# Optimization experiments

Measured on AMD Instinct MI355X. Metric: run time of the kernel, lower is better.

## Reference

```python
import jax, jax.numpy as jnp
import numpy as np

L, H, C, T, V = 6, 6, 384, 256, 65  # n_layer, n_head, n_embd, block_size, vocab_size
DH = C // H                          # head_size = 64
FF = 4 * C                           # 1536
B = 256


def _ln(x, g, b):
    m = x.mean(-1, keepdims=True)
    v = ((x - m) ** 2).mean(-1, keepdims=True)
    return (x - m) * jax.lax.rsqrt(v + 1e-5) * g + b


def setup_inputs() -> dict:
    key = jax.random.key(0)
    ks = jax.random.split(key, 24)
    s = 0.02
    n = lambda k, shp: jax.random.normal(k, shp, dtype=jnp.float32) * s
    return {
        "idx": jax.random.randint(ks[0], (B, T), 0, V),
        "targets": jax.random.randint(ks[1], (B, T), 0, V),
        "tok_emb": n(ks[2], (V, C)),
        "pos_emb": n(ks[3], (T, C)),
        "Wq": n(ks[4], (L, C, C)),
        "Wk": n(ks[5], (L, C, C)),
        "Wv": n(ks[6], (L, C, C)),
        "Wo": n(ks[7], (L, C, C)),
        "bo": jnp.zeros((L, C), jnp.float32),
        "ln1_g": jnp.ones((L, C), jnp.float32),
        "ln1_b": jnp.zeros((L, C), jnp.float32),
        "ln2_g": jnp.ones((L, C), jnp.float32),
        "ln2_b": jnp.zeros((L, C), jnp.float32),
        "W1": n(ks[8], (L, C, FF)),
        "b1": jnp.zeros((L, FF), jnp.float32),
        "W2": n(ks[9], (L, FF, C)),
        "b2": jnp.zeros((L, C), jnp.float32),
        "lnf_g": jnp.ones((C,), jnp.float32),
        "lnf_b": jnp.zeros((C,), jnp.float32),
        "Wh": n(ks[10], (C, V)),
        "bh": jnp.zeros((V,), jnp.float32),
    }


def _forward(idx, targets, tok_emb, pos_emb, Wq, Wk, Wv, Wo, bo,
             ln1_g, ln1_b, ln2_g, ln2_b, W1, b1, W2, b2, lnf_g, lnf_b, Wh, bh):
    Bx, Tx = idx.shape
    x = tok_emb[idx] + pos_emb[:Tx]                       # [B,T,C]
    causal = jnp.tril(jnp.ones((Tx, Tx), bool))

    def block(x, p):
        wq, wk, wv, wo, bo_, g1, b1_, g2, b2_, w1, bf1, w2, bf2 = p
        h = _ln(x, g1, b1_)
        q = (h @ wq).reshape(Bx, Tx, H, DH).transpose(0, 2, 1, 3)   # [B,H,T,Dh]
        k = (h @ wk).reshape(Bx, Tx, H, DH).transpose(0, 2, 1, 3)
        v = (h @ wv).reshape(Bx, Tx, H, DH).transpose(0, 2, 1, 3)
        scores = jnp.einsum('bhqd,bhkd->bhqk', q, k) * (DH ** -0.5)
        scores = jnp.where(causal, scores, -jnp.inf)
        att = jax.nn.softmax(scores, axis=-1)                       # dropout = eval (identity)
        o = jnp.einsum('bhqk,bhkd->bhqd', att, v)
        o = o.transpose(0, 2, 1, 3).reshape(Bx, Tx, C)
        x = x + o @ wo + bo_
        h2 = _ln(x, g2, b2_)
        x = x + jax.nn.relu(h2 @ w1 + bf1) @ w2 + bf2
        return x, None

    x, _ = jax.lax.scan(block, x, (Wq, Wk, Wv, Wo, bo, ln1_g, ln1_b,
                                   ln2_g, ln2_b, W1, b1, W2, b2))
    x = _ln(x, lnf_g, lnf_b)
    logits = (x @ Wh + bh).reshape(Bx * Tx, V)
    logp = jax.nn.log_softmax(logits, axis=-1)
    loss = -logp[jnp.arange(Bx * Tx), targets.reshape(-1)].mean()
    return logits, loss


def reference(idx, targets, tok_emb, pos_emb, Wq, Wk, Wv, Wo, bo,
              ln1_g, ln1_b, ln2_g, ln2_b, W1, b1, W2, b2, lnf_g, lnf_b, Wh, bh):
    return _forward(idx, targets, tok_emb, pos_emb, Wq, Wk, Wv, Wo, bo,
                    ln1_g, ln1_b, ln2_g, ln2_b, W1, b1, W2, b2, lnf_g, lnf_b, Wh, bh)
```

## Files before the change

kernel.cpp:

```cpp
#include <hip/hip_runtime.h>
#include <stdint.h>


typedef unsigned short u16;
typedef unsigned int   u32;
typedef __attribute__((ext_vector_type(8))) short bf16x8;
typedef __attribute__((ext_vector_type(4))) float f32x4;

typedef const __attribute__((address_space(1))) void* gas_ptr;
typedef __attribute__((address_space(3))) void* lds_ptr;

__device__ __forceinline__ void gld_lds16(const void* g, void* l) {
    __builtin_amdgcn_global_load_lds((gas_ptr)g, (lds_ptr)l, 16, 0, 0);
}

__device__ __forceinline__ u16 f2bf(float f) {
    u32 u = __builtin_bit_cast(u32, f);
    u = u + 0x7fffu + ((u >> 16) & 1u);
    return (u16)(u >> 16);
}
__device__ __forceinline__ float bf2f(u16 h) { return __builtin_bit_cast(float, (u32)h << 16); }
__device__ __forceinline__ float bflo(u32 u) { return __builtin_bit_cast(float, u << 16); }
__device__ __forceinline__ float bfhi(u32 u) { return __builtin_bit_cast(float, u & 0xffff0000u); }

__global__ __launch_bounds__(256)
void convT_k(const float* __restrict__ src, u16* __restrict__ dst,
             int L, int R, int C, int dls, int dco)
{
    size_t total  = (size_t)L * R * C;
    size_t stride = (size_t)gridDim.x * 256;
    for (size_t i = (size_t)blockIdx.x * 256 + threadIdx.x; i < total; i += stride) {
        size_t rc  = (size_t)R * C;
        size_t l   = i / rc;
        size_t rem = i - l * rc;
        int r = (int)(rem / C);
        int c = (int)(rem - (size_t)r * C);
        dst[l * (size_t)dls + (size_t)(dco + c) * R + r] = f2bf(src[i]);
    }
}

__global__ __launch_bounds__(256)
void embed_k(const int* __restrict__ idx, const float* __restrict__ tok,
             const float* __restrict__ pos, u16* __restrict__ x,
             float* __restrict__ lossbuf)
{
    if (blockIdx.x == 0 && threadIdx.x < 32) lossbuf[threadIdx.x] = 0.f;
    int gi  = blockIdx.x * 256 + threadIdx.x;
    int row = gi / 48;
    int cg  = gi - row * 48;
    int t   = row & 255;
    const float4* ta = (const float4*)(tok + (size_t)idx[row] * 384 + cg * 8);
    const float4* pa = (const float4*)(pos + (size_t)t * 384 + cg * 8);
    float4 a0 = ta[0], a1 = ta[1], p0 = pa[0], p1 = pa[1];
    u16 o[8] = { f2bf(a0.x+p0.x), f2bf(a0.y+p0.y), f2bf(a0.z+p0.z), f2bf(a0.w+p0.w),
                 f2bf(a1.x+p1.x), f2bf(a1.y+p1.y), f2bf(a1.z+p1.z), f2bf(a1.w+p1.w) };
    *(uint4*)(x + (size_t)row * 384 + cg * 8) = *(uint4*)o;
}

__global__ __launch_bounds__(256)
void ln_k(const u16* __restrict__ x, const float* __restrict__ gg,
          const float* __restrict__ bb, u16* __restrict__ out)
{
    const int lane = threadIdx.x & 63;
    const int w    = threadIdx.x >> 6;
    const size_t row = (size_t)blockIdx.x * 4 + w;
    const u32* xr = (const u32*)(x + row * 384);
    u32 d[3] = { xr[lane], xr[64 + lane], xr[128 + lane] };
    float v[6];
#pragma unroll
    for (int k = 0; k < 3; ++k) { v[2*k] = bflo(d[k]); v[2*k+1] = bfhi(d[k]); }
    float s = 0.f, sq = 0.f;
#pragma unroll
    for (int j = 0; j < 6; ++j) { s += v[j]; sq += v[j]*v[j]; }
#pragma unroll
    for (int m = 1; m < 64; m <<= 1) { s += __shfl_xor(s, m); sq += __shfl_xor(sq, m); }
    float mean = s * (1.f / 384.f);
    float var  = sq * (1.f / 384.f) - mean * mean;
    float rs   = rsqrtf(var + 1e-5f);
    u32* orow = (u32*)(out + row * 384);
#pragma unroll
    for (int k = 0; k < 3; ++k) {
        int c = k * 128 + 2 * lane;
        float o0 = (v[2*k]   - mean) * rs * gg[c]   + bb[c];
        float o1 = (v[2*k+1] - mean) * rs * gg[c+1] + bb[c+1];
        orow[k*64 + lane] = (u32)f2bf(o0) | ((u32)f2bf(o1) << 16);
    }
}

template<int EPI>
__global__ __launch_bounds__(256)
void gemm_bt(const u16* __restrict__ A, const u16* __restrict__ Bt,
             u16* __restrict__ C, float* __restrict__ Cf,
             const float* __restrict__ bias, int K, int N)
{
    __shared__ u16 As[2][128*32];
    __shared__ u16 Bs[2][128*32];
    const int tid = threadIdx.x;
    const int lane = tid & 63;
    const int w  = tid >> 6;
    const int wm = w >> 1, wn = w & 1;

    const int ntn = (N + 127) >> 7;
    const int cpx = gridDim.x >> 3;
    const int swz = (blockIdx.x & 7) * cpx + (blockIdx.x >> 3);
    const int mt  = swz / ntn;
    const int m0  = mt * 128;
    const int n0  = (swz - mt * ntn) * 128;

    const int g   = lane >> 4;
    const int l15 = lane & 15;

    f32x4 acc[4][4] = {};
    const int nk = K >> 5;

    auto stage = [&](int buf, int t) {
        const int k0 = t << 5;
#pragma unroll
        for (int c = 0; c < 2; ++c) {
            int i   = c * 256 + tid;
            int row = i >> 2;
            int seg = (i & 3) ^ (row & 3);
            gld_lds16(A  + (size_t)(m0 + row) * K + k0 + seg * 8,
                      (char*)(&As[buf][0]) + (c * 256 + w * 64) * 16);
            gld_lds16(Bt + (size_t)(n0 + row) * K + k0 + seg * 8,
                      (char*)(&Bs[buf][0]) + (c * 256 + w * 64) * 16);
        }
    };

    stage(0, 0);
    __syncthreads();
    int cur = 0;
    for (int t = 0; t < nk; ++t) {
        if (t + 1 < nk) stage(cur ^ 1, t + 1);
        const char* Ab = (const char*)&As[cur][0];
        const char* Bb = (const char*)&Bs[cur][0];
        bf16x8 af[4], bfv[4];
#pragma unroll
        for (int fm = 0; fm < 4; ++fm) {
            int row = wm*64 + fm*16 + l15;
            af[fm] = *(const bf16x8*)(Ab + row*64 + ((g ^ (row & 3)) * 16));
        }
#pragma unroll
        for (int fn = 0; fn < 4; ++fn) {
            int row = wn*64 + fn*16 + l15;
            bfv[fn] = *(const bf16x8*)(Bb + row*64 + ((g ^ (row & 3)) * 16));
        }
#pragma unroll
        for (int fm = 0; fm < 4; ++fm)
#pragma unroll
            for (int fn = 0; fn < 4; ++fn)
                acc[fm][fn] = __builtin_amdgcn_mfma_f32_16x16x32_bf16(
                    af[fm], bfv[fn], acc[fm][fn], 0, 0, 0);
        __syncthreads();
        cur ^= 1;
    }

#pragma unroll
    for (int fm = 0; fm < 4; ++fm) {
        int rowb = m0 + wm*64 + fm*16 + g*4;
#pragma unroll
        for (int fn = 0; fn < 4; ++fn) {
            int col = n0 + wn*64 + fn*16 + l15;
            float bv = (EPI == 0) ? 0.f
                     : ((EPI == 3 && col >= N) ? 0.f : bias[col]);
#pragma unroll
            for (int r = 0; r < 4; ++r) {
                size_t off = (size_t)(rowb + r) * N + col;
                float vv = acc[fm][fn][r];
                if (EPI == 0) {
                    C[off] = f2bf(vv);
                } else if (EPI == 1) {
                    vv += bv; vv = vv > 0.f ? vv : 0.f;
                    C[off] = f2bf(vv);
                } else if (EPI == 2) {
                    C[off] = f2bf(bf2f(C[off]) + vv + bv);
                } else {
                    if (col < N) Cf[off] = vv + bv;
                }
            }
        }
    }
}

__global__ __launch_bounds__(256)
void attn_k(const u16* __restrict__ qkv, u16* __restrict__ op)
{
    __shared__ u16 Ks[256*64];
    __shared__ u16 Vt[64*256];
    __shared__ u16 Ps[4][64*64];
    const int tid  = threadIdx.x;
    const int lane = tid & 63;
    const int w    = tid >> 6;
    const int g    = lane >> 4;
    const int l15  = lane & 15;
    const int bh = blockIdx.x;
    const int b  = bh / 6, hh = bh - b * 6;
    const size_t baseQ = (size_t)b * 256 * 1152 + hh * 64;
    const size_t baseK = baseQ + 384;
    const size_t baseV = baseQ + 768;

#pragma unroll
    for (int cc = 0; cc < 8; ++cc) {
        int i    = cc * 256 + tid;
        int row  = i >> 3;
        int slot = (i & 7) ^ (row & 7);
        gld_lds16(qkv + baseK + (size_t)row * 1152 + slot * 8,
                  (char*)Ks + (cc * 256 + w * 64) * 16);
    }
#pragma unroll
    for (int it = 0; it < 16; ++it) {
        int j    = it * 256 + tid;
        int trow = j >> 4;
        int d0   = (j & 15) * 4;
        uint2 val = *(const uint2*)(qkv + baseV + (size_t)trow * 1152 + d0);
        u16 e0 = (u16)(val.x & 0xffff), e1 = (u16)(val.x >> 16);
        u16 e2 = (u16)(val.y & 0xffff), e3 = (u16)(val.y >> 16);
        *(u16*)((char*)Vt + (d0+0)*512 + ((trow*2) ^ (((d0+0)&7) << 4))) = e0;
        *(u16*)((char*)Vt + (d0+1)*512 + ((trow*2) ^ (((d0+1)&7) << 4))) = e1;
        *(u16*)((char*)Vt + (d0+2)*512 + ((trow*2) ^ (((d0+2)&7) << 4))) = e2;
        *(u16*)((char*)Vt + (d0+3)*512 + ((trow*2) ^ (((d0+3)&7) << 4))) = e3;
    }
    __syncthreads();

    const int r0 = w * 64;
    bf16x8 qf[4][2];
#pragma unroll
    for (int fm = 0; fm < 4; ++fm)
#pragma unroll
        for (int kk = 0; kk < 2; ++kk)
            qf[fm][kk] = *(const bf16x8*)(qkv + baseQ +
                (size_t)(r0 + fm*16 + l15) * 1152 + kk*32 + g*8);

    f32x4 oacc[4][4] = {};
    float mst[4][4], lst[4][4];
#pragma unroll
    for (int i = 0; i < 4; ++i)
#pragma unroll
        for (int r = 0; r < 4; ++r) { mst[i][r] = -1e30f; lst[i][r] = 0.f; }

    for (int kt = 0; kt <= w; ++kt) {
        f32x4 s[4][4] = {};
#pragma unroll
        for (int kk = 0; kk < 2; ++kk) {
            bf16x8 kf[4];
#pragma unroll
            for (int fn = 0; fn < 4; ++fn) {
                int row = kt*64 + fn*16 + l15;
                kf[fn] = *(const bf16x8*)((char*)Ks + row*128 +
                          ((kk*64 + g*16) ^ ((row & 7) << 4)));
            }
#pragma unroll
            for (int fm = 0; fm < 4; ++fm)
#pragma unroll
                for (int fn = 0; fn < 4; ++fn)
                    s[fm][fn] = __builtin_amdgcn_mfma_f32_16x16x32_bf16(
                        qf[fm][kk], kf[fn], s[fm][fn], 0, 0, 0);
        }
        const bool diag = (kt == w);
#pragma unroll
        for (int fm = 0; fm < 4; ++fm) {
#pragma unroll
            for (int r = 0; r < 4; ++r) {
                int rowg = r0 + fm*16 + g*4 + r;
                float mx = -1e30f;
#pragma unroll
                for (int fn = 0; fn < 4; ++fn) {
                    float val = s[fm][fn][r] * 0.125f;
                    if (diag) {
                        int colg = kt*64 + fn*16 + l15;
                        if (colg > rowg) val = -1e30f;
                    }
                    s[fm][fn][r] = val;
                    mx = fmaxf(mx, val);
                }
                mx = fmaxf(mx, __shfl_xor(mx, 1));
                mx = fmaxf(mx, __shfl_xor(mx, 2));
                mx = fmaxf(mx, __shfl_xor(mx, 4));
                mx = fmaxf(mx, __shfl_xor(mx, 8));
                float mnew = fmaxf(mst[fm][r], mx);
                float sf   = __expf(mst[fm][r] - mnew);
                mst[fm][r] = mnew;
                float rowsum = 0.f;
#pragma unroll
                for (int fn = 0; fn < 4; ++fn) {
                    float pe = __expf(s[fm][fn][r] - mnew);
                    s[fm][fn][r] = pe;
                    rowsum += pe;
                }
                rowsum += __shfl_xor(rowsum, 1);
                rowsum += __shfl_xor(rowsum, 2);
                rowsum += __shfl_xor(rowsum, 4);
                rowsum += __shfl_xor(rowsum, 8);
                lst[fm][r] = lst[fm][r] * sf + rowsum;
#pragma unroll
                for (int fd = 0; fd < 4; ++fd) oacc[fm][fd][r] *= sf;
                int prow = fm*16 + g*4 + r;
#pragma unroll
                for (int fn = 0; fn < 4; ++fn) {
                    int pcol = fn*16 + l15;
                    *(u16*)((char*)Ps[w] + prow*128 +
                            ((pcol*2) ^ ((prow & 7) << 4))) = f2bf(s[fm][fn][r]);
                }
            }
        }
        asm volatile("s_waitcnt lgkmcnt(0)" ::: "memory");
#pragma unroll
        for (int kk2 = 0; kk2 < 2; ++kk2) {
            bf16x8 pa[4], vb[4];
#pragma unroll
            for (int fm = 0; fm < 4; ++fm) {
                int prow = fm*16 + l15;
                pa[fm] = *(const bf16x8*)((char*)Ps[w] + prow*128 +
                          ((kk2*64 + g*16) ^ ((prow & 7) << 4)));
            }
#pragma unroll
            for (int fd = 0; fd < 4; ++fd) {
                int vrow = fd*16 + l15;
                vb[fd] = *(const bf16x8*)((char*)Vt + vrow*512 +
                          ((kt*128 + kk2*64 + g*16) ^ ((vrow & 7) << 4)));
            }
#pragma unroll
            for (int fm = 0; fm < 4; ++fm)
#pragma unroll
                for (int fd = 0; fd < 4; ++fd)
                    oacc[fm][fd] = __builtin_amdgcn_mfma_f32_16x16x32_bf16(
                        pa[fm], vb[fd], oacc[fm][fd], 0, 0, 0);
        }
    }
#pragma unroll
    for (int fm = 0; fm < 4; ++fm)
#pragma unroll
        for (int r = 0; r < 4; ++r) {
            int rowg = r0 + fm*16 + g*4 + r;
            float inv = 1.f / lst[fm][r];
#pragma unroll
            for (int fd = 0; fd < 4; ++fd)
                op[((size_t)b * 256 + rowg) * 384 + hh*64 + fd*16 + l15] =
                    f2bf(oacc[fm][fd][r] * inv);
        }
}

__global__ __launch_bounds__(256)
void loss_k(const float* __restrict__ logits, const int* __restrict__ tgt,
            float* __restrict__ lossbuf)
{
    __shared__ float wloss[4];
    const int lane = threadIdx.x & 63;
    const int w    = threadIdx.x >> 6;
    const int wid  = blockIdx.x * 4 + w;
    float acc = 0.f;
    for (int rr = 0; rr < 16; ++rr) {
        const size_t row = (size_t)wid * 16 + rr;
        const float* lr = logits + row * 65;
        float v   = lr[lane];
        float l64 = lr[64];
        float mx = fmaxf(v, l64);
#pragma unroll
        for (int m = 1; m < 64; m <<= 1) mx = fmaxf(mx, __shfl_xor(mx, m));
        float e = __expf(v - mx);
#pragma unroll
        for (int m = 1; m < 64; m <<= 1) e += __shfl_xor(e, m);
        e += __expf(l64 - mx);
        float lse = mx + logf(e);
        int t = tgt[row];
        float lt0 = __shfl(v, t < 64 ? t : 0);
        float lt  = (t < 64) ? lt0 : l64;
        acc += lse - lt;
    }
    if (lane == 0) wloss[w] = acc;
    __syncthreads();
    if (threadIdx.x == 0) {
        float bsum = wloss[0] + wloss[1] + wloss[2] + wloss[3];
        atomicAdd(&lossbuf[blockIdx.x & 31], bsum * (1.f / 65536.f));
    }
}

__global__ void loss_finish_k(const float* __restrict__ part, float* __restrict__ outp)
{
    int lane = threadIdx.x;
    float v = (lane < 32) ? part[lane] : 0.f;
#pragma unroll
    for (int m = 1; m < 64; m <<= 1) v += __shfl_xor(v, m);
    if (lane == 0) outp[0] = v;
}

extern "C" void kernel_launch(void* const* d_in, const int* in_sizes, int n_in,
                              void* d_out, int out_size, void* d_ws, size_t ws_size,
                              hipStream_t stream)
{
    (void)in_sizes; (void)n_in; (void)out_size;
    const int*   idx  = (const int*)d_in[0];
    const int*   tgt  = (const int*)d_in[1];
    const float* tok  = (const float*)d_in[2];
    const float* pos  = (const float*)d_in[3];
    const float* Wq   = (const float*)d_in[4];
    const float* Wk   = (const float*)d_in[5];
    const float* Wv   = (const float*)d_in[6];
    const float* Wo   = (const float*)d_in[7];
    const float* bo   = (const float*)d_in[8];
    const float* ln1g = (const float*)d_in[9];
    const float* ln1b = (const float*)d_in[10];
    const float* ln2g = (const float*)d_in[11];
    const float* ln2b = (const float*)d_in[12];
    const float* W1   = (const float*)d_in[13];
    const float* b1   = (const float*)d_in[14];
    const float* W2   = (const float*)d_in[15];
    const float* b2   = (const float*)d_in[16];
    const float* lnfg = (const float*)d_in[17];
    const float* lnfb = (const float*)d_in[18];
    const float* Wh   = (const float*)d_in[19];
    const float* bh   = (const float*)d_in[20];

    const size_t fixed = (size_t)65536*384*2 * 2
                       + (size_t)6*1152*384*2
                       + (size_t)6*384*384*2
                       + (size_t)6*1536*384*2 * 2
                       + (size_t)128*384*2 + 4096;
    int NC = 4;
    if      (ws_size >= fixed + (size_t)65536*1536*2)      NC = 1;
    else if (ws_size >= fixed + (size_t)32768*1536*2)      NC = 2;
    const int CR = 65536 / NC;

    char* p = (char*)d_ws;
    u16* x    = (u16*)p;  p += (size_t)65536*384*2;
    u16* hbuf = (u16*)p;  p += (size_t)65536*384*2;
    u16* r1   = (u16*)p;  p += (size_t)CR*1536*2;
    u16* wqkv = (u16*)p;  p += (size_t)6*1152*384*2;
    u16* wto  = (u16*)p;  p += (size_t)6*384*384*2;
    u16* wt1  = (u16*)p;  p += (size_t)6*1536*384*2;
    u16* wt2  = (u16*)p;  p += (size_t)6*384*1536*2;
    u16* wth  = (u16*)p;  p += (size_t)128*384*2;
    float* lossbuf = (float*)p;

    float* out   = (float*)d_out;
    float* lossp = out + (size_t)65536 * 65;

    convT_k<<<1024, 256, 0, stream>>>(Wq, wqkv, 6, 384, 384, 442368, 0);
    convT_k<<<1024, 256, 0, stream>>>(Wk, wqkv, 6, 384, 384, 442368, 384);
    convT_k<<<1024, 256, 0, stream>>>(Wv, wqkv, 6, 384, 384, 442368, 768);
    convT_k<<<1024, 256, 0, stream>>>(Wo, wto, 6, 384, 384, 147456, 0);
    convT_k<<<2048, 256, 0, stream>>>(W1, wt1, 6, 384, 1536, 589824, 0);
    convT_k<<<2048, 256, 0, stream>>>(W2, wt2, 6, 1536, 384, 589824, 0);
    convT_k<<<64,   256, 0, stream>>>(Wh, wth, 1, 384, 65, 24960, 0);

    embed_k<<<12288, 256, 0, stream>>>(idx, tok, pos, x, lossbuf);

    for (int l = 0; l < 6; ++l) {
        ln_k<<<16384, 256, 0, stream>>>(x, ln1g + l*384, ln1b + l*384, hbuf);
        for (int ac = 0; ac < NC; ++ac) {
            const size_t ro = (size_t)ac * CR;
            gemm_bt<0><<<dim3((CR/128)*9), 256, 0, stream>>>(
                hbuf + ro*384, wqkv + (size_t)l*442368, r1, nullptr, nullptr, 384, 1152);
            attn_k<<<(CR/256)*6, 256, 0, stream>>>(r1, hbuf + ro*384);
        }
        gemm_bt<2><<<dim3(512*3), 256, 0, stream>>>(
            hbuf, wto + (size_t)l*147456, x, nullptr, bo + l*384, 384, 384);
        ln_k<<<16384, 256, 0, stream>>>(x, ln2g + l*384, ln2b + l*384, hbuf);
        for (int mc = 0; mc < NC; ++mc) {
            const size_t ro = (size_t)mc * CR;
            gemm_bt<1><<<dim3((CR/128)*12), 256, 0, stream>>>(
                hbuf + ro*384, wt1 + (size_t)l*589824, r1, nullptr, b1 + l*1536, 384, 1536);
            gemm_bt<2><<<dim3((CR/128)*3), 256, 0, stream>>>(
                r1, wt2 + (size_t)l*589824, x + ro*384, nullptr, b2 + l*384, 1536, 384);
        }
    }
    ln_k<<<16384, 256, 0, stream>>>(x, lnfg, lnfb, hbuf);
    gemm_bt<3><<<dim3(512), 256, 0, stream>>>(
        hbuf, wth, nullptr, out, bh, 384, 65);
    loss_k<<<1024, 256, 0, stream>>>(out, tgt, lossbuf);
    loss_finish_k<<<1, 64, 0, stream>>>(lossbuf, lossp);
}
```

Before: 3.839 ms.

## Split attention into 8 waves of 32 rows with balanced causal pairing

The attention kernel now runs 512 threads, and each of its 8 waves handles 32 query rows instead of 64. Waves are paired (w and 11-w) so the causal work is spread more evenly across the block. The V transpose and P buffers switch from XOR swizzling to padded row strides, and the V load becomes scalar 2-byte global reads. This trades more waves and lower per-wave register use for better load balance, at the risk of slower uncoalesced V loads and higher LDS use.

```diff
diff --git a/kernel.cpp b/kernel.cpp
--- a/kernel.cpp
+++ b/kernel.cpp
@@ -182,12 +182,12 @@
     }
 }
 
-__global__ __launch_bounds__(256)
+__global__ __launch_bounds__(512, 2)
 void attn_k(const u16* __restrict__ qkv, u16* __restrict__ op)
 {
     __shared__ u16 Ks[256*64];
-    __shared__ u16 Vt[64*256];
-    __shared__ u16 Ps[4][64*64];
+    __shared__ u16 Vt[64*264];
+    __shared__ u16 Ps[8][32*72];
     const int tid  = threadIdx.x;
     const int lane = tid & 63;
     const int w    = tid >> 6;
@@ -200,46 +200,50 @@
     const size_t baseV = baseQ + 768;
 
 #pragma unroll
-    for (int cc = 0; cc < 8; ++cc) {
-        int i    = cc * 256 + tid;
+    for (int cc = 0; cc < 4; ++cc) {
+        int i    = cc * 512 + tid;
         int row  = i >> 3;
         int slot = (i & 7) ^ (row & 7);
         gld_lds16(qkv + baseK + (size_t)row * 1152 + slot * 8,
-                  (char*)Ks + (cc * 256 + w * 64) * 16);
-    }
-#pragma unroll
-    for (int it = 0; it < 16; ++it) {
-        int j    = it * 256 + tid;
-        int trow = j >> 4;
-        int d0   = (j & 15) * 4;
-        uint2 val = *(const uint2*)(qkv + baseV + (size_t)trow * 1152 + d0);
-        u16 e0 = (u16)(val.x & 0xffff), e1 = (u16)(val.x >> 16);
-        u16 e2 = (u16)(val.y & 0xffff), e3 = (u16)(val.y >> 16);
-        *(u16*)((char*)Vt + (d0+0)*512 + ((trow*2) ^ (((d0+0)&7) << 4))) = e0;
-        *(u16*)((char*)Vt + (d0+1)*512 + ((trow*2) ^ (((d0+1)&7) << 4))) = e1;
-        *(u16*)((char*)Vt + (d0+2)*512 + ((trow*2) ^ (((d0+2)&7) << 4))) = e2;
-        *(u16*)((char*)Vt + (d0+3)*512 + ((trow*2) ^ (((d0+3)&7) << 4))) = e3;
+                  (char*)Ks + (cc * 512 + w * 64) * 16);
+    }
+#pragma unroll
+    for (int it = 0; it < 8; ++it) {
+        int j = it * 512 + tid;
+        int q = j & 15;
+        int t = j >> 4;
+        const u16* vrow = qkv + baseV + (size_t)t * 1152;
+#pragma unroll
+        for (int m = 0; m < 4; ++m) {
+            int d = q + 16 * m;
+            *(u16*)((char*)Vt + d * 528 + t * 2) = vrow[d];
+        }
     }
     __syncthreads();
 
-    const int r0 = w * 64;
-    bf16x8 qf[4][2];
-#pragma unroll
-    for (int fm = 0; fm < 4; ++fm)
+    const int rb = (w < 4) ? w : 11 - w;
+    const int r0 = rb * 32;
+    const int ktmax = rb >> 1;
+
+    bf16x8 qf[2][2];
+#pragma unroll
+    for (int fm = 0; fm < 2; ++fm)
 #pragma unroll
         for (int kk = 0; kk < 2; ++kk)
             qf[fm][kk] = *(const bf16x8*)(qkv + baseQ +
                 (size_t)(r0 + fm*16 + l15) * 1152 + kk*32 + g*8);
 
-    f32x4 oacc[4][4] = {};
-    float mst[4][4], lst[4][4];
-#pragma unroll
-    for (int i = 0; i < 4; ++i)
+    f32x4 oacc[2][4] = {};
+    float mst[2][4], lst[2][4];
+#pragma unroll
+    for (int i = 0; i < 2; ++i)
 #pragma unroll
         for (int r = 0; r < 4; ++r) { mst[i][r] = -1e30f; lst[i][r] = 0.f; }
 
-    for (int kt = 0; kt <= w; ++kt) {
-        f32x4 s[4][4] = {};
+    char* Pw = (char*)Ps[w];
+
+    for (int kt = 0; kt <= ktmax; ++kt) {
+        f32x4 s[2][4] = {};
 #pragma unroll
         for (int kk = 0; kk < 2; ++kk) {
             bf16x8 kf[4];
@@ -250,15 +254,15 @@
                           ((kk*64 + g*16) ^ ((row & 7) << 4)));
             }
 #pragma unroll
-            for (int fm = 0; fm < 4; ++fm)
+            for (int fm = 0; fm < 2; ++fm)
 #pragma unroll
                 for (int fn = 0; fn < 4; ++fn)
                     s[fm][fn] = __builtin_amdgcn_mfma_f32_16x16x32_bf16(
                         qf[fm][kk], kf[fn], s[fm][fn], 0, 0, 0);
         }
-        const bool diag = (kt == w);
-#pragma unroll
-        for (int fm = 0; fm < 4; ++fm) {
+        const bool diag = (kt == ktmax);
+#pragma unroll
+        for (int fm = 0; fm < 2; ++fm) {
 #pragma unroll
             for (int r = 0; r < 4; ++r) {
                 int rowg = r0 + fm*16 + g*4 + r;
@@ -298,29 +302,27 @@
 #pragma unroll
                 for (int fn = 0; fn < 4; ++fn) {
                     int pcol = fn*16 + l15;
-                    *(u16*)((char*)Ps[w] + prow*128 +
-                            ((pcol*2) ^ ((prow & 7) << 4))) = f2bf(s[fm][fn][r]);
+                    *(u16*)(Pw + prow*144 + pcol*2) = f2bf(s[fm][fn][r]);
                 }
             }
         }
         asm volatile("s_waitcnt lgkmcnt(0)" ::: "memory");
 #pragma unroll
         for (int kk2 = 0; kk2 < 2; ++kk2) {
-            bf16x8 pa[4], vb[4];
-#pragma unroll
-            for (int fm = 0; fm < 4; ++fm) {
+            bf16x8 pa[2], vb[4];
+#pragma unroll
+            for (int fm = 0; fm < 2; ++fm) {
                 int prow = fm*16 + l15;
-                pa[fm] = *(const bf16x8*)((char*)Ps[w] + prow*128 +
-                          ((kk2*64 + g*16) ^ ((prow & 7) << 4)));
+                pa[fm] = *(const bf16x8*)(Pw + prow*144 + kk2*64 + g*16);
             }
 #pragma unroll
             for (int fd = 0; fd < 4; ++fd) {
                 int vrow = fd*16 + l15;
-                vb[fd] = *(const bf16x8*)((char*)Vt + vrow*512 +
-                          ((kt*128 + kk2*64 + g*16) ^ ((vrow & 7) << 4)));
+                vb[fd] = *(const bf16x8*)((char*)Vt + vrow*528 +
+                          kt*128 + kk2*64 + g*16);
             }
 #pragma unroll
-            for (int fm = 0; fm < 4; ++fm)
+            for (int fm = 0; fm < 2; ++fm)
 #pragma unroll
                 for (int fd = 0; fd < 4; ++fd)
                     oacc[fm][fd] = __builtin_amdgcn_mfma_f32_16x16x32_bf16(
@@ -328,7 +330,7 @@
         }
     }
 #pragma unroll
-    for (int fm = 0; fm < 4; ++fm)
+    for (int fm = 0; fm < 2; ++fm)
 #pragma unroll
         for (int r = 0; r < 4; ++r) {
             int rowg = r0 + fm*16 + g*4 + r;
@@ -451,7 +453,7 @@
             const size_t ro = (size_t)ac * CR;
             gemm_bt<0><<<dim3((CR/128)*9), 256, 0, stream>>>(
                 hbuf + ro*384, wqkv + (size_t)l*442368, r1, nullptr, nullptr, 384, 1152);
-            attn_k<<<(CR/256)*6, 256, 0, stream>>>(r1, hbuf + ro*384);
+            attn_k<<<(CR/256)*6, 512, 0, stream>>>(r1, hbuf + ro*384);
         }
         gemm_bt<2><<<dim3(512*3), 256, 0, stream>>>(
             hbuf, wto + (size_t)l*147456, x, nullptr, bo + l*384, 384, 384);
```

New measurement: 3.350 ms. 1.15x faster.
